# Performance work log

Hardware: AMD Instinct MI355X
Metric: run time of the kernel (lower is better)

The kernel has to match this reference:

```python
import jax, jax.numpy as jnp
import numpy as np

NEG_SLOPE = 0.01  # LeakyReLU default
STRIDE = 5        # group_length // 4
EPS = 1e-5        # RMSNorm eps


def leaky_relu(x):
    return jnp.where(x >= 0, x, NEG_SLOPE * x)


def rmsnorm(x, w):
    return x * jax.lax.rsqrt(jnp.mean(x * x, axis=-1, keepdims=True) + EPS) * w


def s6(x, fc1_w, fc1_b, fc2_w, fc2_b, fc3_w, fc3_b, A):
    # x: [B, L, D] with D = 2*d_model; A: [D, N]
    delta = jax.nn.softplus(x @ fc1_w.T + fc1_b)        # [B, L, D]
    Bm = x @ fc2_w.T + fc2_b                             # [B, L, N]
    Cm = x @ fc3_w.T + fc3_b                             # [B, L, N]
    dA = jnp.exp(jnp.einsum('bld,dn->bldn', delta, A))   # [B, L, D, N]
    dBx = jnp.einsum('bld,bln,bld->bldn', delta, Bm, x)  # delta * B * x

    def step(h, inp):
        dA_t, dBx_t = inp
        h = dA_t * h + dBx_t
        return h, h

    B_, L, D, N = dA.shape
    h0 = jnp.zeros((B_, D, N), dtype=x.dtype)
    _, hs = jax.lax.scan(step, h0, (jnp.swapaxes(dA, 0, 1), jnp.swapaxes(dBx, 0, 1)))
    hs = jnp.swapaxes(hs, 0, 1)                          # [B, L, D, N]
    return jnp.einsum('bln,bldn->bld', Cm, hs)           # [B, L, D]


def setup_inputs() -> dict:
    key = jax.random.key(0)
    ks = iter(jax.random.split(key, 32))

    def rn(shape, scale=0.02):
        return scale * jax.random.normal(next(ks), shape, dtype=jnp.float32)

    B, band, gl, d, N, L = 256, 189, 20, 128, 128, 34
    di = 2 * d
    return {
        'x': jax.random.normal(next(ks), (B, 1, band), dtype=jnp.float32),
        'conv_w': rn((d, 1, gl)), 'conv_b': rn((d,)),
        'norm_w': jnp.ones((d,), jnp.float32),
        'inp_w': rn((di, d)), 'inp_b': rn((di,)),
        'seqconv_w': rn((L, L, 3)), 'seqconv_b': rn((L,)),
        'convlin_w': rn((di, di)), 'convlin_b': rn((di,)),
        'fc1_w': rn((di, di)), 'fc1_b': rn((di,)),
        'fc2_w': rn((N, di)), 'fc2_b': rn((N,)),
        'fc3_w': rn((N, di)), 'fc3_b': rn((N,)),
        'A': jnp.ones((di, N), jnp.float32) / jnp.sqrt(jnp.float32(N)),
        'D_w': rn((di, d)), 'D_b': rn((di,)),
        'out_w': rn((d, di)), 'out_b': rn((d,)),
        'fnn1_w': rn((64, L * d)), 'fnn1_b': rn((64,)),
        'fnn2_w': rn((32, 64)), 'fnn2_b': rn((32,)),
    }


def reference(x, conv_w, conv_b, norm_w, inp_w, inp_b, seqconv_w, seqconv_b,
              convlin_w, convlin_b, fc1_w, fc1_b, fc2_w, fc2_b, fc3_w, fc3_b,
              A, D_w, D_b, out_w, out_b, fnn1_w, fnn1_b, fnn2_w, fnn2_b):
    # group division: Conv1d(1, d, k=20, stride=5) + LeakyReLU
    g = jax.lax.conv_general_dilated(x, conv_w, (STRIDE,), [(0, 0)],
                                     dimension_numbers=('NCH', 'OIH', 'NCH'))
    g = leaky_relu(g + conv_b[None, :, None])            # [B, d, L]
    h = jnp.swapaxes(g, 1, 2)                            # [B, L, d]
    # Mamba block
    xn = rmsnorm(h, norm_w)
    xp = xn @ inp_w.T + inp_b                            # [B, L, 2d]
    # Conv1d(seq_len, seq_len, k=3, pad=1): seq axis L is the channel dim
    xc = jax.lax.conv_general_dilated(xp, seqconv_w, (1,), [(1, 1)],
                                      dimension_numbers=('NCH', 'OIH', 'NCH'))
    xc = jax.nn.silu(xc + seqconv_b[None, :, None])
    xc = xc @ convlin_w.T + convlin_b                    # [B, L, 2d]
    xs = s6(xc, fc1_w, fc1_b, fc2_w, fc2_b, fc3_w, fc3_b, A)
    y = jax.nn.silu(xs) * jax.nn.silu(xn @ D_w.T + D_b)  # gated
    y = y @ out_w.T + out_b                              # [B, L, d]
    # FNN head
    f = y.reshape(y.shape[0], -1)                        # [B, L*d]
    f = leaky_relu(f @ fnn1_w.T + fnn1_b)
    return f @ fnn2_w.T + fnn2_b                         # [B, 32]
```

## Files before the change

### kernel.cpp

```cpp
#include <hip/hip_runtime.h>
#include <math.h>


#define NB    256
#define LL    34
#define DD    128
#define DI    256
#define NN    128
#define MM    (NB*LL)

using u16 = unsigned short;
typedef __attribute__((ext_vector_type(8))) short short8;
typedef __attribute__((ext_vector_type(4))) float f32x4;

__device__ __forceinline__ float silu_f(float x)  { return x / (1.f + __expf(-x)); }
__device__ __forceinline__ float softplus_f(float x) {
    return fmaxf(x, 0.f) + __logf(1.f + __expf(-fabsf(x)));
}
__device__ __forceinline__ float leaky_f(float x) { return (x >= 0.f) ? x : 0.01f * x; }

__device__ __forceinline__ u16 f2bf(float x) {
    unsigned u = __float_as_uint(x);
    return (u16)((u + 0x7FFF + ((u >> 16) & 1)) >> 16);
}
__device__ __forceinline__ float bf2f(u16 h) {
    return __uint_as_float(((unsigned)h) << 16);
}
__device__ __forceinline__ void f2pair(float v, u16* h, u16* l) {
    u16 hh = f2bf(v);
    *h = hh;
    *l = f2bf(v - bf2f(hh));
}

__global__ void prep_w_k(const float* __restrict__ inp_w, const float* __restrict__ D_w,
                         const float* __restrict__ fc1_w, const float* __restrict__ fc2_w,
                         const float* __restrict__ fc3_w, const float* __restrict__ convlin_w,
                         const float* __restrict__ out_w,
                         const float* __restrict__ inp_b, const float* __restrict__ D_b,
                         const float* __restrict__ fc1_b, const float* __restrict__ fc2_b,
                         const float* __restrict__ fc3_b,
                         u16* __restrict__ wc1h, u16* __restrict__ wc1l,
                         u16* __restrict__ wc3h, u16* __restrict__ wc3l,
                         u16* __restrict__ cvh,  u16* __restrict__ cvl,
                         u16* __restrict__ owh,  u16* __restrict__ owl,
                         float* __restrict__ bias1, float* __restrict__ bias3)
{
    int i = blockIdx.x * 256 + threadIdx.x;
    if (i < 65536) {
        float v = (i < 32768) ? inp_w[i] : D_w[i - 32768];
        f2pair(v, &wc1h[i], &wc1l[i]);
    } else if (i < 196608) {
        int j = i - 65536;
        float v = (j < 65536) ? fc1_w[j] : (j < 98304 ? fc2_w[j - 65536] : fc3_w[j - 98304]);
        f2pair(v, &wc3h[j], &wc3l[j]);
    } else if (i < 262144) {
        int j = i - 196608;
        f2pair(convlin_w[j], &cvh[j], &cvl[j]);
    } else if (i < 294912) {
        int j = i - 262144;
        f2pair(out_w[j], &owh[j], &owl[j]);
    }
    if (i < 512)  bias1[i] = (i < 256) ? inp_b[i] : D_b[i - 256];
    else if (i < 1024) {
        int j = i - 512;
        bias3[j] = (j < 256) ? fc1_b[j] : (j < 384 ? fc2_b[j - 256] : fc3_b[j - 384]);
    }
}

__global__ __launch_bounds__(256)
void check_uni_k(const float* __restrict__ A, int* __restrict__ flag)
{
    const int tid = threadIdx.x;
    __shared__ int s;
    if (tid == 0) s = 1;
    __syncthreads();
    bool ok = true;
    for (int k = 0; k < 128; k++) {
        int idx = tid + k * 256;
        ok &= (A[idx] == A[idx & ~127]);
    }
    if (!ok) s = 0;
    __syncthreads();
    if (tid == 0) *flag = s;
}

__global__ __launch_bounds__(256)
void transpose_k(const float* __restrict__ W1, float* __restrict__ W1T)
{
    __shared__ float tile[64][65];
    const int bx = blockIdx.x;
    const int tid = threadIdx.x;
    for (int p = 0; p < 16; p++) {
        int idx = tid + p * 256;
        int r = idx >> 6, c = idx & 63;
        tile[r][c] = W1[(size_t)r * 4352 + bx * 64 + c];
    }
    __syncthreads();
    for (int p = 0; p < 16; p++) {
        int idx = tid + p * 256;
        int cc = idx >> 6, rr = idx & 63;
        W1T[(size_t)(bx * 64 + cc) * 64 + rr] = tile[rr][cc];
    }
}

__global__ __launch_bounds__(128)
void conv_norm_k(const float* __restrict__ x, const float* __restrict__ cw,
                 const float* __restrict__ cb, const float* __restrict__ nw,
                 u16* __restrict__ XNh, u16* __restrict__ XNl)
{
    int bl = blockIdx.x;
    int b = bl / LL, l = bl % LL;
    int c = threadIdx.x;
    const float* xr = x + (size_t)b * 189 + l * 5;
    float g = cb[c];
    #pragma unroll
    for (int k = 0; k < 20; k++) g = fmaf(xr[k], cw[c * 20 + k], g);
    g = leaky_f(g);

    float s = g * g;
    #pragma unroll
    for (int m = 32; m >= 1; m >>= 1) s += __shfl_xor(s, m);
    __shared__ float wsum[2];
    if ((threadIdx.x & 63) == 0) wsum[threadIdx.x >> 6] = s;
    __syncthreads();
    float mean = (wsum[0] + wsum[1]) * (1.f / 128.f);
    float inv = 1.f / sqrtf(mean + 1e-5f);
    float v = g * inv * nw[c];
    f2pair(v, &XNh[(size_t)bl * DD + c], &XNl[(size_t)bl * DD + c]);
}

template <int K, int EPI>
__global__ __launch_bounds__(256)
void mgemm_k(const u16* __restrict__ Ah, const u16* __restrict__ Al,
             const u16* __restrict__ Wh, const u16* __restrict__ Wl,
             const float* __restrict__ bias,
             float* __restrict__ Y, int ldy,
             u16* __restrict__ Yh, u16* __restrict__ Yl)
{
    const int tid  = threadIdx.x;
    const int r0   = blockIdx.x * 128;
    const int c0   = blockIdx.y * 64;
    const int wave = tid >> 6;
    const int lane = tid & 63;
    const int wm   = wave & 1;
    const int wn   = wave >> 1;
    const int l15  = lane & 15;
    const int lq   = lane >> 4;

    __shared__ u16 sAh[128][40];
    __shared__ u16 sAl[128][40];
    __shared__ u16 sBh[64][40];
    __shared__ u16 sBl[64][40];

    f32x4 acc[4][2];
    #pragma unroll
    for (int i = 0; i < 4; i++)
        #pragma unroll
        for (int j = 0; j < 2; j++) acc[i][j] = (f32x4){0.f, 0.f, 0.f, 0.f};

    const int a_row = tid >> 1;
    const int a_kb  = (tid & 1) * 16;
    const int b_row = tid >> 2;
    const int b_ko  = (tid & 3) * 8;

    for (int k0 = 0; k0 < K; k0 += 32) {
        const u16* ga = Ah + (size_t)(r0 + a_row) * K + k0 + a_kb;
        const u16* gl = Al + (size_t)(r0 + a_row) * K + k0 + a_kb;
        short8 vh0 = *(const short8*)(ga);
        short8 vh1 = *(const short8*)(ga + 8);
        short8 vl0 = *(const short8*)(gl);
        short8 vl1 = *(const short8*)(gl + 8);
        const u16* gb = Wh + (size_t)(c0 + b_row) * K + k0 + b_ko;
        const u16* gc = Wl + (size_t)(c0 + b_row) * K + k0 + b_ko;
        short8 wb = *(const short8*)(gb);
        short8 wc = *(const short8*)(gc);

        *(short8*)&sAh[a_row][a_kb]     = vh0;
        *(short8*)&sAh[a_row][a_kb + 8] = vh1;
        *(short8*)&sAl[a_row][a_kb]     = vl0;
        *(short8*)&sAl[a_row][a_kb + 8] = vl1;
        *(short8*)&sBh[b_row][b_ko] = wb;
        *(short8*)&sBl[b_row][b_ko] = wc;
        __syncthreads();

        short8 fah[4], fal[4], fbh[2], fbl[2];
        #pragma unroll
        for (int i = 0; i < 4; i++) {
            fah[i] = *(const short8*)&sAh[wm * 64 + i * 16 + l15][lq * 8];
            fal[i] = *(const short8*)&sAl[wm * 64 + i * 16 + l15][lq * 8];
        }
        #pragma unroll
        for (int j = 0; j < 2; j++) {
            fbh[j] = *(const short8*)&sBh[wn * 32 + j * 16 + l15][lq * 8];
            fbl[j] = *(const short8*)&sBl[wn * 32 + j * 16 + l15][lq * 8];
        }
        #pragma unroll
        for (int i = 0; i < 4; i++)
            #pragma unroll
            for (int j = 0; j < 2; j++) {
                acc[i][j] = __builtin_amdgcn_mfma_f32_16x16x32_bf16(fah[i], fbh[j], acc[i][j], 0, 0, 0);
                acc[i][j] = __builtin_amdgcn_mfma_f32_16x16x32_bf16(fah[i], fbl[j], acc[i][j], 0, 0, 0);
                acc[i][j] = __builtin_amdgcn_mfma_f32_16x16x32_bf16(fal[i], fbh[j], acc[i][j], 0, 0, 0);
            }
        __syncthreads();
    }

    #pragma unroll
    for (int i = 0; i < 4; i++) {
        int gr = r0 + wm * 64 + i * 16 + lq * 4;
        #pragma unroll
        for (int j = 0; j < 2; j++) {
            int gc = c0 + wn * 32 + j * 16 + l15;
            float bb = bias[gc];
            #pragma unroll
            for (int r = 0; r < 4; r++) {
                float v = acc[i][j][r] + bb;
                if (EPI == 1) { if (gc < 256) v = softplus_f(v); }
                if (EPI == 2) {
                    u16 hh, ll;
                    f2pair(v, &hh, &ll);
                    Yh[(size_t)(gr + r) * ldy + gc] = hh;
                    Yl[(size_t)(gr + r) * ldy + gc] = ll;
                } else {
                    Y[(size_t)(gr + r) * ldy + gc] = v;
                }
            }
        }
    }
}

__global__ __launch_bounds__(256)
void seqconv_k(const float* __restrict__ XP, int ldxp,
               const float* __restrict__ w, const float* __restrict__ bias,
               u16* __restrict__ XCh, u16* __restrict__ XCl)
{
    const int b   = blockIdx.x;
    const int tid = threadIdx.x;
    const int tx  = tid & 63;
    const int ty  = tid >> 6;
    const int j0  = tx * 4;

    __shared__ float sx[LL][264];
    __shared__ float sw[LL][112];

    for (int idx = tid; idx < LL * 256; idx += 256) {
        int li = idx >> 8, jj = idx & 255;
        sx[li][jj + 1] = XP[(size_t)(b * LL + li) * ldxp + jj];
    }
    if (tid < LL) { sx[tid][0] = 0.f; sx[tid][257] = 0.f; }
    for (int idx = tid; idx < LL * LL * 3; idx += 256) {
        int lo = idx / 102;
        int rem = idx - lo * 102;
        int li = rem / 3;
        int k  = rem - li * 3;
        sw[li][lo * 3 + k] = w[idx];
    }
    __syncthreads();

    const int base = ty * 9 - (ty == 3 ? 1 : 0);
    const int cnt  = (ty < 2) ? 9 : 8;

    float acc[9][4];
    #pragma unroll
    for (int i = 0; i < 9; i++)
        #pragma unroll
        for (int jj = 0; jj < 4; jj++) acc[i][jj] = 0.f;

    for (int li = 0; li < LL; li++) {
        float4 xa = *(const float4*)&sx[li][j0];
        float2 xb = *(const float2*)&sx[li][j0 + 4];
        float xv[6] = {xa.x, xa.y, xa.z, xa.w, xb.x, xb.y};
        const float* swr = &sw[li][0];
        #pragma unroll
        for (int i = 0; i < 9; i++) {
            if (i < cnt) {
                int lo3 = (base + i) * 3;
                float w0 = swr[lo3 + 0];
                float w1 = swr[lo3 + 1];
                float w2 = swr[lo3 + 2];
                #pragma unroll
                for (int jj = 0; jj < 4; jj++) {
                    acc[i][jj] = fmaf(w0, xv[jj],     acc[i][jj]);
                    acc[i][jj] = fmaf(w1, xv[jj + 1], acc[i][jj]);
                    acc[i][jj] = fmaf(w2, xv[jj + 2], acc[i][jj]);
                }
            }
        }
    }

    #pragma unroll
    for (int i = 0; i < 9; i++) {
        if (i < cnt) {
            int lo = base + i;
            float bb = bias[lo];
            ushort4 oh, ol;
            float v0 = silu_f(acc[i][0] + bb);
            float v1 = silu_f(acc[i][1] + bb);
            float v2 = silu_f(acc[i][2] + bb);
            float v3 = silu_f(acc[i][3] + bb);
            f2pair(v0, &oh.x, &ol.x);
            f2pair(v1, &oh.y, &ol.y);
            f2pair(v2, &oh.z, &ol.z);
            f2pair(v3, &oh.w, &ol.w);
            size_t o = (size_t)(b * LL + lo) * DI + j0;
            *(ushort4*)&XCh[o] = oh;
            *(ushort4*)&XCl[o] = ol;
        }
    }
}

__global__ __launch_bounds__(256)
void ssd_scan_k(const int* __restrict__ flag,
                const float* __restrict__ dBC,
                const u16* __restrict__ Xh, const u16* __restrict__ Xl,
                const float* __restrict__ A,
                const float* __restrict__ DG,
                u16* __restrict__ Gh, u16* __restrict__ Gl)
{
    if (*flag == 0) return;
    const int b   = blockIdx.x;
    const int tid = threadIdx.x;
    const int lane = tid & 63;

    __shared__ float sB[LL][132];
    __shared__ float sC[LL][132];
    __shared__ float sM[LL][36];

    const float* rowbase = dBC + (size_t)b * LL * 512;
    for (int idx = tid; idx < LL * 128; idx += 256) {
        int l = idx >> 7, n = idx & 127;
        sB[l][n] = rowbase[l * 512 + 256 + n];
        sC[l][n] = rowbase[l * 512 + 384 + n];
    }
    __syncthreads();

    for (int e = tid; e < LL * LL; e += 256) {
        int l = e / LL, t = e - l * LL;
        if (t <= l) {
            float acc = 0.f;
            #pragma unroll
            for (int kk = 0; kk < 32; kk++) {
                int k = ((lane + kk) & 31) * 4;
                float4 vb = *(const float4*)&sB[t][k];
                float4 vc = *(const float4*)&sC[l][k];
                acc += vb.x * vc.x + vb.y * vc.y + vb.z * vc.z + vb.w * vc.w;
            }
            sM[l][t] = acc;
        }
    }
    __syncthreads();

    const int d = tid;
    const float a_d = A[(size_t)d * NN];
    const float* pDel = rowbase + d;
    const u16* pXh = Xh + (size_t)b * LL * 256 + d;
    const u16* pXl = Xl + (size_t)b * LL * 256 + d;

    float u[LL], eS[LL];
    float S = 0.f;
    #pragma unroll
    for (int l = 0; l < LL; l++) {
        float dl = pDel[l * 512];
        S = fmaf(dl, a_d, S);
        eS[l] = __expf(S);
        float xv = bf2f(pXh[l * 256]) + bf2f(pXl[l * 256]);
        u[l] = __expf(-S) * dl * xv;
    }

    const float* pG = DG + (size_t)b * LL * 512 + 256 + d;
    u16* pGh = Gh + (size_t)b * LL * 256 + d;
    u16* pGl = Gl + (size_t)b * LL * 256 + d;
    #pragma unroll
    for (int l = 0; l < LL; l++) {
        float acc = 0.f;
        for (int t = 0; t <= l; t++) acc = fmaf(sM[l][t], u[t], acc);
        float xs = eS[l] * acc;
        float g = silu_f(xs) * silu_f(pG[l * 512]);
        u16 hh, ll2;
        f2pair(g, &hh, &ll2);
        pGh[l * 256] = hh;
        pGl[l * 256] = ll2;
    }
}

__global__ __launch_bounds__(256)
void scan_fb_k(const int* __restrict__ flag,
               const float* __restrict__ dBC,
               const u16*  __restrict__ Xh, const u16* __restrict__ Xl,
               const float* __restrict__ A,
               const float* __restrict__ DG,
               u16* __restrict__ Gh, u16* __restrict__ Gl)
{
    if (*flag != 0) return;
    const int b  = blockIdx.y;
    const int d0 = blockIdx.x * 64;
    const int tid = threadIdx.x;
    const int sub = tid & 15;
    const int pg  = tid >> 4;
    const int dbase = d0 + pg * 4;
    const int nA = sub * 4;

    float a[4][8], h[4][8];
    #pragma unroll
    for (int dd = 0; dd < 4; dd++) {
        const float* Ar = A + (size_t)(dbase + dd) * NN;
        float4 q0 = *(const float4*)(Ar + nA);
        float4 q1 = *(const float4*)(Ar + 64 + nA);
        a[dd][0]=q0.x; a[dd][1]=q0.y; a[dd][2]=q0.z; a[dd][3]=q0.w;
        a[dd][4]=q1.x; a[dd][5]=q1.y; a[dd][6]=q1.z; a[dd][7]=q1.w;
        #pragma unroll
        for (int j = 0; j < 8; j++) h[dd][j] = 0.f;
    }

    const float* pD  = dBC + (size_t)b * LL * 512 + dbase;
    const float* pBC = dBC + (size_t)b * LL * 512 + 256 + nA;
    const u16*  pXh = Xh  + (size_t)b * LL * 256 + dbase;
    const u16*  pXl = Xl  + (size_t)b * LL * 256 + dbase;
    const float* pG  = DG  + (size_t)b * LL * 512 + 256 + dbase;
    u16* pGh = Gh + (size_t)b * LL * 256 + dbase;
    u16* pGl = Gl + (size_t)b * LL * 256 + dbase;

    for (int l = 0; l < LL; l++) {
        float4  cD  = *(const float4*)(pD);
        ushort4 cXh = *(const ushort4*)(pXh);
        ushort4 cXl = *(const ushort4*)(pXl);
        float4 cB0 = *(const float4*)(pBC);
        float4 cB1 = *(const float4*)(pBC + 64);
        float4 cC0 = *(const float4*)(pBC + 128);
        float4 cC1 = *(const float4*)(pBC + 192);
        pD += 512; pBC += 512; pXh += 256; pXl += 256;

        float xv[4] = { bf2f(cXh.x) + bf2f(cXl.x), bf2f(cXh.y) + bf2f(cXl.y),
                        bf2f(cXh.z) + bf2f(cXl.z), bf2f(cXh.w) + bf2f(cXl.w) };
        float dl[4] = {cD.x, cD.y, cD.z, cD.w};
        float dx[4] = {cD.x * xv[0], cD.y * xv[1], cD.z * xv[2], cD.w * xv[3]};
        float bv[8] = {cB0.x,cB0.y,cB0.z,cB0.w,cB1.x,cB1.y,cB1.z,cB1.w};
        float cv[8] = {cC0.x,cC0.y,cC0.z,cC0.w,cC1.x,cC1.y,cC1.z,cC1.w};

        float accd[4] = {0.f, 0.f, 0.f, 0.f};
        #pragma unroll
        for (int dd = 0; dd < 4; dd++)
            #pragma unroll
            for (int j = 0; j < 8; j++) {
                float dA = __expf(dl[dd] * a[dd][j]);
                h[dd][j] = fmaf(dA, h[dd][j], dx[dd] * bv[j]);
                accd[dd] = fmaf(cv[j], h[dd][j], accd[dd]);
            }
        #pragma unroll
        for (int dd = 0; dd < 4; dd++) {
            float v = accd[dd];
            v += __shfl_xor(v, 1);
            v += __shfl_xor(v, 2);
            v += __shfl_xor(v, 4);
            v += __shfl_xor(v, 8);
            accd[dd] = v;
        }
        if (sub == 0) {
            float4 dg = *(const float4*)(pG);
            ushort4 oh, ol;
            float g0 = silu_f(accd[0]) * silu_f(dg.x);
            float g1 = silu_f(accd[1]) * silu_f(dg.y);
            float g2 = silu_f(accd[2]) * silu_f(dg.z);
            float g3 = silu_f(accd[3]) * silu_f(dg.w);
            f2pair(g0, &oh.x, &ol.x);
            f2pair(g1, &oh.y, &ol.y);
            f2pair(g2, &oh.z, &ol.z);
            f2pair(g3, &oh.w, &ol.w);
            *(ushort4*)pGh = oh;
            *(ushort4*)pGl = ol;
        }
        pG += 512; pGh += 256; pGl += 256;
    }
}

__global__ __launch_bounds__(256)
void fnn1_k(const float* __restrict__ F, const float* __restrict__ W1T,
            float* __restrict__ partials)
{
    const int btile = blockIdx.x;
    const int kc    = blockIdx.y;
    const int tid   = threadIdx.x;
    __shared__ float sf[16][260];
    for (int i = tid; i < 16 * 256; i += 256) {
        int r = i >> 8, c = i & 255;
        sf[r][c] = F[(size_t)(btile * 16 + r) * 4352 + kc * 256 + c];
    }
    __syncthreads();

    const int o  = tid & 63;
    const int bq = tid >> 6;
    const float* w = W1T + (size_t)(kc * 256) * 64 + o;
    float acc[4] = {0.f, 0.f, 0.f, 0.f};
    for (int k = 0; k < 256; k += 4) {
        float w0 = w[(size_t)(k + 0) * 64];
        float w1 = w[(size_t)(k + 1) * 64];
        float w2 = w[(size_t)(k + 2) * 64];
        float w3 = w[(size_t)(k + 3) * 64];
        #pragma unroll
        for (int bj = 0; bj < 4; bj++) {
            float4 f4 = *(const float4*)&sf[bq * 4 + bj][k];
            acc[bj] = fmaf(w0, f4.x, acc[bj]);
            acc[bj] = fmaf(w1, f4.y, acc[bj]);
            acc[bj] = fmaf(w2, f4.z, acc[bj]);
            acc[bj] = fmaf(w3, f4.w, acc[bj]);
        }
    }
    #pragma unroll
    for (int bj = 0; bj < 4; bj++)
        partials[(size_t)kc * 16384 + (btile * 16 + bq * 4 + bj) * 64 + o] = acc[bj];
}

__global__ __launch_bounds__(64)
void fnn2_k(const float* __restrict__ partials,
            const float* __restrict__ B1,
            const float* __restrict__ W2, const float* __restrict__ B2,
            float* __restrict__ out)
{
    int b = blockIdx.x;
    int t = threadIdx.x;
    __shared__ float s1[64];
    float acc = B1[t];
    #pragma unroll
    for (int kc = 0; kc < 17; kc++)
        acc += partials[(size_t)kc * 16384 + b * 64 + t];
    s1[t] = leaky_f(acc);
    __syncthreads();

    if (t < 32) {
        float acc2 = B2[t];
        const float* w2 = W2 + t * 64;
        #pragma unroll
        for (int j = 0; j < 64; j++) acc2 = fmaf(s1[j], w2[j], acc2);
        out[(size_t)b * 32 + t] = acc2;
    }
}

extern "C" void kernel_launch(void* const* d_in, const int* in_sizes, int n_in,
                              void* d_out, int out_size, void* d_ws, size_t ws_size,
                              hipStream_t stream)
{
    const float* x        = (const float*)d_in[0];
    const float* conv_w   = (const float*)d_in[1];
    const float* conv_b   = (const float*)d_in[2];
    const float* norm_w   = (const float*)d_in[3];
    const float* inp_w    = (const float*)d_in[4];
    const float* inp_b    = (const float*)d_in[5];
    const float* seqconv_w= (const float*)d_in[6];
    const float* seqconv_b= (const float*)d_in[7];
    const float* convlin_w= (const float*)d_in[8];
    const float* convlin_b= (const float*)d_in[9];
    const float* fc1_w    = (const float*)d_in[10];
    const float* fc1_b    = (const float*)d_in[11];
    const float* fc2_w    = (const float*)d_in[12];
    const float* fc2_b    = (const float*)d_in[13];
    const float* fc3_w    = (const float*)d_in[14];
    const float* fc3_b    = (const float*)d_in[15];
    const float* A        = (const float*)d_in[16];
    const float* D_w      = (const float*)d_in[17];
    const float* D_b      = (const float*)d_in[18];
    const float* out_w    = (const float*)d_in[19];
    const float* out_b    = (const float*)d_in[20];
    const float* fnn1_w   = (const float*)d_in[21];
    const float* fnn1_b   = (const float*)d_in[22];
    const float* fnn2_w   = (const float*)d_in[23];
    const float* fnn2_b   = (const float*)d_in[24];

    char* W = (char*)d_ws;
    float* buf1  = (float*)(W + 0);
    float* buf3  = (float*)(W + 17825792);
    u16*   xnh   = (u16*)  (W + 35651584);
    u16*   xnl   = (u16*)  (W + 37879808);
    u16*   xc2h  = (u16*)  (W + 35651584);
    float* fout  = (float*)(W + 35651584);
    u16*   xc2l  = (u16*)  (W + 40108032);
    u16*   xch   = (u16*)  (W + 44564480);
    u16*   xcl   = (u16*)  (W + 49020928);
    float* w1t   = (float*)(W + 53477376);
    u16*   wc1h  = (u16*)  (W + 54591488);
    u16*   wc1l  = (u16*)  (W + 54722560);
    u16*   wc3h  = (u16*)  (W + 54853632);
    u16*   wc3l  = (u16*)  (W + 55115776);
    u16*   cvh   = (u16*)  (W + 55377920);
    u16*   cvl   = (u16*)  (W + 55508992);
    u16*   owh   = (u16*)  (W + 55640064);
    u16*   owl   = (u16*)  (W + 55705600);
    float* bias1 = (float*)(W + 55771136);
    float* bias3 = (float*)(W + 55773184);
    int*   uflag = (int*)  (W + 55775232);
    u16* gateh = xch;
    u16* gatel = xcl;
    float* partials = buf3;

    prep_w_k<<<1152, 256, 0, stream>>>(inp_w, D_w, fc1_w, fc2_w, fc3_w,
                                       convlin_w, out_w,
                                       inp_b, D_b, fc1_b, fc2_b, fc3_b,
                                       wc1h, wc1l, wc3h, wc3l, cvh, cvl,
                                       owh, owl, bias1, bias3);
    check_uni_k<<<1, 256, 0, stream>>>(A, uflag);
    transpose_k<<<68, 256, 0, stream>>>(fnn1_w, w1t);

    conv_norm_k<<<MM, 128, 0, stream>>>(x, conv_w, conv_b, norm_w, xnh, xnl);

    mgemm_k<128, 0><<<dim3(MM / 128, 8), 256, 0, stream>>>(
        xnh, xnl, wc1h, wc1l, bias1, buf1, 512, nullptr, nullptr);

    seqconv_k<<<NB, 256, 0, stream>>>(buf1, 512, seqconv_w, seqconv_b, xch, xcl);

    mgemm_k<256, 2><<<dim3(MM / 128, 4), 256, 0, stream>>>(
        xch, xcl, cvh, cvl, convlin_b, nullptr, 256, xc2h, xc2l);

    mgemm_k<256, 1><<<dim3(MM / 128, 8), 256, 0, stream>>>(
        xc2h, xc2l, wc3h, wc3l, bias3, buf3, 512, nullptr, nullptr);

    ssd_scan_k<<<NB, 256, 0, stream>>>(uflag, buf3, xc2h, xc2l, A, buf1,
                                       gateh, gatel);
    scan_fb_k<<<dim3(4, NB), 256, 0, stream>>>(uflag, buf3, xc2h, xc2l, A,
                                               buf1, gateh, gatel);

    mgemm_k<256, 0><<<dim3(MM / 128, 2), 256, 0, stream>>>(
        gateh, gatel, owh, owl, out_b, fout, 128, nullptr, nullptr);

    fnn1_k<<<dim3(16, 17), 256, 0, stream>>>(fout, w1t, partials);
    fnn2_k<<<NB, 64, 0, stream>>>(partials, fnn1_b, fnn2_w, fnn2_b,
                                  (float*)d_out);
}
```

Baseline: 228.9 us.

## Merge prep kernels and compute scan C·Bᵀ matrix with split-bf16 MFMA

```diff
diff --git a/kernel.cpp b/kernel.cpp
--- a/kernel.cpp
+++ b/kernel.cpp
@@ -32,74 +32,72 @@
     *l = f2bf(v - bf2f(hh));
 }
 
-__global__ void prep_w_k(const float* __restrict__ inp_w, const float* __restrict__ D_w,
-                         const float* __restrict__ fc1_w, const float* __restrict__ fc2_w,
-                         const float* __restrict__ fc3_w, const float* __restrict__ convlin_w,
-                         const float* __restrict__ out_w,
-                         const float* __restrict__ inp_b, const float* __restrict__ D_b,
-                         const float* __restrict__ fc1_b, const float* __restrict__ fc2_b,
-                         const float* __restrict__ fc3_b,
-                         u16* __restrict__ wc1h, u16* __restrict__ wc1l,
-                         u16* __restrict__ wc3h, u16* __restrict__ wc3l,
-                         u16* __restrict__ cvh,  u16* __restrict__ cvl,
-                         u16* __restrict__ owh,  u16* __restrict__ owl,
-                         float* __restrict__ bias1, float* __restrict__ bias3)
-{
-    int i = blockIdx.x * 256 + threadIdx.x;
-    if (i < 65536) {
-        float v = (i < 32768) ? inp_w[i] : D_w[i - 32768];
-        f2pair(v, &wc1h[i], &wc1l[i]);
-    } else if (i < 196608) {
-        int j = i - 65536;
-        float v = (j < 65536) ? fc1_w[j] : (j < 98304 ? fc2_w[j - 65536] : fc3_w[j - 98304]);
-        f2pair(v, &wc3h[j], &wc3l[j]);
-    } else if (i < 262144) {
-        int j = i - 196608;
-        f2pair(convlin_w[j], &cvh[j], &cvl[j]);
-    } else if (i < 294912) {
-        int j = i - 262144;
-        f2pair(out_w[j], &owh[j], &owl[j]);
-    }
-    if (i < 512)  bias1[i] = (i < 256) ? inp_b[i] : D_b[i - 256];
-    else if (i < 1024) {
-        int j = i - 512;
-        bias3[j] = (j < 256) ? fc1_b[j] : (j < 384 ? fc2_b[j - 256] : fc3_b[j - 384]);
-    }
-}
-
 __global__ __launch_bounds__(256)
-void check_uni_k(const float* __restrict__ A, int* __restrict__ flag)
-{
+void prep_all_k(const float* __restrict__ inp_w, const float* __restrict__ D_w,
+                const float* __restrict__ fc1_w, const float* __restrict__ fc2_w,
+                const float* __restrict__ fc3_w, const float* __restrict__ convlin_w,
+                const float* __restrict__ out_w,
+                const float* __restrict__ inp_b, const float* __restrict__ D_b,
+                const float* __restrict__ fc1_b, const float* __restrict__ fc2_b,
+                const float* __restrict__ fc3_b,
+                const float* __restrict__ W1, const float* __restrict__ A,
+                u16* __restrict__ wc1h, u16* __restrict__ wc1l,
+                u16* __restrict__ wc3h, u16* __restrict__ wc3l,
+                u16* __restrict__ cvh,  u16* __restrict__ cvl,
+                u16* __restrict__ owh,  u16* __restrict__ owl,
+                float* __restrict__ bias1, float* __restrict__ bias3,
+                float* __restrict__ W1T, int* __restrict__ flag)
+{
+    const int bx  = blockIdx.x;
     const int tid = threadIdx.x;
-    __shared__ int s;
-    if (tid == 0) s = 1;
-    __syncthreads();
-    bool ok = true;
-    for (int k = 0; k < 128; k++) {
-        int idx = tid + k * 256;
-        ok &= (A[idx] == A[idx & ~127]);
-    }
-    if (!ok) s = 0;
-    __syncthreads();
-    if (tid == 0) *flag = s;
-}
-
-__global__ __launch_bounds__(256)
-void transpose_k(const float* __restrict__ W1, float* __restrict__ W1T)
-{
     __shared__ float tile[64][65];
-    const int bx = blockIdx.x;
-    const int tid = threadIdx.x;
-    for (int p = 0; p < 16; p++) {
-        int idx = tid + p * 256;
-        int r = idx >> 6, c = idx & 63;
-        tile[r][c] = W1[(size_t)r * 4352 + bx * 64 + c];
-    }
-    __syncthreads();
-    for (int p = 0; p < 16; p++) {
-        int idx = tid + p * 256;
-        int cc = idx >> 6, rr = idx & 63;
-        W1T[(size_t)(bx * 64 + cc) * 64 + rr] = tile[rr][cc];
+
+    if (bx < 1152) {
+        int i = bx * 256 + tid;
+        if (i < 65536) {
+            float v = (i < 32768) ? inp_w[i] : D_w[i - 32768];
+            f2pair(v, &wc1h[i], &wc1l[i]);
+        } else if (i < 196608) {
+            int j = i - 65536;
+            float v = (j < 65536) ? fc1_w[j] : (j < 98304 ? fc2_w[j - 65536] : fc3_w[j - 98304]);
+            f2pair(v, &wc3h[j], &wc3l[j]);
+        } else if (i < 262144) {
+            int j = i - 196608;
+            f2pair(convlin_w[j], &cvh[j], &cvl[j]);
+        } else if (i < 294912) {
+            int j = i - 262144;
+            f2pair(out_w[j], &owh[j], &owl[j]);
+        }
+        if (i < 512)  bias1[i] = (i < 256) ? inp_b[i] : D_b[i - 256];
+        else if (i < 1024) {
+            int j = i - 512;
+            bias3[j] = (j < 256) ? fc1_b[j] : (j < 384 ? fc2_b[j - 256] : fc3_b[j - 384]);
+        }
+    } else if (bx < 1220) {
+        const int bt = bx - 1152;
+        for (int p = 0; p < 16; p++) {
+            int idx = tid + p * 256;
+            int r = idx >> 6, c = idx & 63;
+            tile[r][c] = W1[(size_t)r * 4352 + bt * 64 + c];
+        }
+        __syncthreads();
+        for (int p = 0; p < 16; p++) {
+            int idx = tid + p * 256;
+            int cc = idx >> 6, rr = idx & 63;
+            W1T[(size_t)(bt * 64 + cc) * 64 + rr] = tile[rr][cc];
+        }
+    } else {
+        __shared__ int s;
+        if (tid == 0) s = 1;
+        __syncthreads();
+        bool ok = true;
+        for (int k = 0; k < 128; k++) {
+            int idx = tid + k * 256;
+            ok &= (A[idx] == A[idx & ~127]);
+        }
+        if (!ok) s = 0;
+        __syncthreads();
+        if (tid == 0) *flag = s;
     }
 }
 
@@ -135,7 +133,8 @@
              const u16* __restrict__ Wh, const u16* __restrict__ Wl,
              const float* __restrict__ bias,
              float* __restrict__ Y, int ldy,
-             u16* __restrict__ Yh, u16* __restrict__ Yl)
+             u16* __restrict__ Yh, u16* __restrict__ Yl,
+             u16* __restrict__ BC)
 {
     const int tid  = threadIdx.x;
     const int r0   = blockIdx.x * 128;
@@ -215,7 +214,7 @@
             #pragma unroll
             for (int r = 0; r < 4; r++) {
                 float v = acc[i][j][r] + bb;
-                if (EPI == 1) { if (gc < 256) v = softplus_f(v); }
+                if (EPI == 1 || EPI == 3) { if (gc < 256) v = softplus_f(v); }
                 if (EPI == 2) {
                     u16 hh, ll;
                     f2pair(v, &hh, &ll);
@@ -223,6 +222,14 @@
                     Yl[(size_t)(gr + r) * ldy + gc] = ll;
                 } else {
                     Y[(size_t)(gr + r) * ldy + gc] = v;
+                    if (EPI == 3 && gc >= 256) {
+                        u16 hh, ll;
+                        f2pair(v, &hh, &ll);
+                        u16* rb = BC + (size_t)(gr + r) * 1024
+                                     + ((gc < 384) ? 0 : 256) + (gc & 127);
+                        rb[0]   = hh;
+                        rb[128] = ll;
+                    }
                 }
             }
         }
@@ -312,47 +319,57 @@
 __global__ __launch_bounds__(256)
 void ssd_scan_k(const int* __restrict__ flag,
                 const float* __restrict__ dBC,
+                const u16* __restrict__ BC,
                 const u16* __restrict__ Xh, const u16* __restrict__ Xl,
                 const float* __restrict__ A,
                 const float* __restrict__ DG,
                 u16* __restrict__ Gh, u16* __restrict__ Gl)
 {
     if (*flag == 0) return;
-    const int b   = blockIdx.x;
-    const int tid = threadIdx.x;
+    const int b    = blockIdx.x;
+    const int tid  = threadIdx.x;
+    const int wave = tid >> 6;
     const int lane = tid & 63;
-
-    __shared__ float sB[LL][132];
-    __shared__ float sC[LL][132];
-    __shared__ float sM[LL][36];
-
-    const float* rowbase = dBC + (size_t)b * LL * 512;
-    for (int idx = tid; idx < LL * 128; idx += 256) {
-        int l = idx >> 7, n = idx & 127;
-        sB[l][n] = rowbase[l * 512 + 256 + n];
-        sC[l][n] = rowbase[l * 512 + 384 + n];
+    const int l15  = lane & 15;
+    const int lq   = lane >> 4;
+
+    __shared__ u16 sBh[48][136], sBl[48][136];
+    __shared__ u16 sCh[48][136], sCl[48][136];
+    __shared__ float sM[48][49];
+
+    const u16* base = BC + (size_t)b * LL * 1024;
+    for (int idx = tid; idx < LL * 16; idx += 256) {
+        int l = idx >> 4, c = (idx & 15) << 3;
+        const u16* row = base + l * 1024;
+        *(short8*)&sBh[l][c] = *(const short8*)&row[c];
+        *(short8*)&sBl[l][c] = *(const short8*)&row[128 + c];
+        *(short8*)&sCh[l][c] = *(const short8*)&row[256 + c];
+        *(short8*)&sCl[l][c] = *(const short8*)&row[384 + c];
     }
     __syncthreads();
 
-    for (int e = tid; e < LL * LL; e += 256) {
-        int l = e / LL, t = e - l * LL;
-        if (t <= l) {
-            float acc = 0.f;
-            #pragma unroll
-            for (int kk = 0; kk < 32; kk++) {
-                int k = ((lane + kk) & 31) * 4;
-                float4 vb = *(const float4*)&sB[t][k];
-                float4 vc = *(const float4*)&sC[l][k];
-                acc += vb.x * vc.x + vb.y * vc.y + vb.z * vc.z + vb.w * vc.w;
-            }
-            sM[l][t] = acc;
-        }
+    for (int tt = wave; tt < 9; tt += 4) {
+        int ti = tt / 3, tj = tt - ti * 3;
+        f32x4 acc = (f32x4){0.f, 0.f, 0.f, 0.f};
+        #pragma unroll
+        for (int ks = 0; ks < 4; ks++) {
+            short8 ch = *(const short8*)&sCh[ti * 16 + l15][ks * 32 + lq * 8];
+            short8 cl = *(const short8*)&sCl[ti * 16 + l15][ks * 32 + lq * 8];
+            short8 bh = *(const short8*)&sBh[tj * 16 + l15][ks * 32 + lq * 8];
+            short8 bl = *(const short8*)&sBl[tj * 16 + l15][ks * 32 + lq * 8];
+            acc = __builtin_amdgcn_mfma_f32_16x16x32_bf16(ch, bh, acc, 0, 0, 0);
+            acc = __builtin_amdgcn_mfma_f32_16x16x32_bf16(ch, bl, acc, 0, 0, 0);
+            acc = __builtin_amdgcn_mfma_f32_16x16x32_bf16(cl, bh, acc, 0, 0, 0);
+        }
+        #pragma unroll
+        for (int r = 0; r < 4; r++)
+            sM[ti * 16 + lq * 4 + r][tj * 16 + l15] = acc[r];
     }
     __syncthreads();
 
     const int d = tid;
     const float a_d = A[(size_t)d * NN];
-    const float* pDel = rowbase + d;
+    const float* pDel = dBC + (size_t)b * LL * 512 + d;
     const u16* pXh = Xh + (size_t)b * LL * 256 + d;
     const u16* pXl = Xl + (size_t)b * LL * 256 + d;
 
@@ -589,36 +606,36 @@
     int*   uflag = (int*)  (W + 55775232);
     u16* gateh = xch;
     u16* gatel = xcl;
+    u16* bcpair = (u16*)buf1;
     float* partials = buf3;
 
-    prep_w_k<<<1152, 256, 0, stream>>>(inp_w, D_w, fc1_w, fc2_w, fc3_w,
-                                       convlin_w, out_w,
-                                       inp_b, D_b, fc1_b, fc2_b, fc3_b,
-                                       wc1h, wc1l, wc3h, wc3l, cvh, cvl,
-                                       owh, owl, bias1, bias3);
-    check_uni_k<<<1, 256, 0, stream>>>(A, uflag);
-    transpose_k<<<68, 256, 0, stream>>>(fnn1_w, w1t);
+    prep_all_k<<<1221, 256, 0, stream>>>(inp_w, D_w, fc1_w, fc2_w, fc3_w,
+                                         convlin_w, out_w,
+                                         inp_b, D_b, fc1_b, fc2_b, fc3_b,
+                                         fnn1_w, A,
+                                         wc1h, wc1l, wc3h, wc3l, cvh, cvl,
+                                         owh, owl, bias1, bias3, w1t, uflag);
 
     conv_norm_k<<<MM, 128, 0, stream>>>(x, conv_w, conv_b, norm_w, xnh, xnl);
 
     mgemm_k<128, 0><<<dim3(MM / 128, 8), 256, 0, stream>>>(
-        xnh, xnl, wc1h, wc1l, bias1, buf1, 512, nullptr, nullptr);
+        xnh, xnl, wc1h, wc1l, bias1, buf1, 512, nullptr, nullptr, nullptr);
 
     seqconv_k<<<NB, 256, 0, stream>>>(buf1, 512, seqconv_w, seqconv_b, xch, xcl);
 
     mgemm_k<256, 2><<<dim3(MM / 128, 4), 256, 0, stream>>>(
-        xch, xcl, cvh, cvl, convlin_b, nullptr, 256, xc2h, xc2l);
-
-    mgemm_k<256, 1><<<dim3(MM / 128, 8), 256, 0, stream>>>(
-        xc2h, xc2l, wc3h, wc3l, bias3, buf3, 512, nullptr, nullptr);
-
-    ssd_scan_k<<<NB, 256, 0, stream>>>(uflag, buf3, xc2h, xc2l, A, buf1,
-                                       gateh, gatel);
+        xch, xcl, cvh, cvl, convlin_b, nullptr, 256, xc2h, xc2l, nullptr);
+
+    mgemm_k<256, 3><<<dim3(MM / 128, 8), 256, 0, stream>>>(
+        xc2h, xc2l, wc3h, wc3l, bias3, buf3, 512, nullptr, nullptr, bcpair);
+
+    ssd_scan_k<<<NB, 256, 0, stream>>>(uflag, buf3, bcpair, xc2h, xc2l, A,
+                                       buf1, gateh, gatel);
     scan_fb_k<<<dim3(4, NB), 256, 0, stream>>>(uflag, buf3, xc2h, xc2l, A,
                                                buf1, gateh, gatel);
 
     mgemm_k<256, 0><<<dim3(MM / 128, 2), 256, 0, stream>>>(
-        gateh, gatel, owh, owl, out_b, fout, 128, nullptr, nullptr);
+        gateh, gatel, owh, owl, out_b, fout, 128, nullptr, nullptr, nullptr);
 
     fnn1_k<<<dim3(16, 17), 256, 0, stream>>>(fout, w1t, partials);
     fnn2_k<<<NB, 64, 0, stream>>>(partials, fnn1_b, fnn2_w, fnn2_b,
```

After: 220.5 us. 1.04x faster.
